# Kernel tuning notes

Hardware: AMD Instinct MI355X
Metric: run time of the kernel (lower is better)

The kernel has to match this reference:

```python
import jax, jax.numpy as jnp
import numpy as np

NUM_PERSISTENT = 16
ALIBI_ALPHA = 1.0
START_I = 0
DILATION = 1
LN_EPS = 1e-5


def setup_inputs() -> dict:
    key = jax.random.key(0)
    ks = jax.random.split(key, 16)
    B, S, C, H = 8, 1024, 512, 8
    D = C // H
    P = NUM_PERSISTENT
    Kk = 3
    x = jax.random.normal(ks[0], (B, S, C), dtype=jnp.float32)
    mask = jnp.ones((B, 1, S, S), dtype=jnp.int32)
    sc = 0.02
    Wq = jax.random.normal(ks[1], (D, D), jnp.float32) * sc
    Wk = jax.random.normal(ks[2], (D, D), jnp.float32) * sc
    Wv = jax.random.normal(ks[3], (D, D), jnp.float32) * sc
    pk = jax.random.normal(ks[4], (P, H, D), jnp.float32) * sc
    pv = jax.random.normal(ks[5], (P, H, D), jnp.float32) * sc
    th_pre = jax.random.normal(ks[6], (H, H), jnp.float32) * (1.0 / np.sqrt(H))
    th_post = jax.random.normal(ks[7], (H, H), jnp.float32) * (1.0 / np.sqrt(H))
    fc_w = jax.random.normal(ks[8], (C, C), jnp.float32) * sc
    fc_b = jnp.zeros((C,), jnp.float32)
    conv1_w = jax.random.normal(ks[9], (C, C, Kk), jnp.float32) * 0.01
    conv1_b = jnp.zeros((C,), jnp.float32)
    conv2_w = jax.random.normal(ks[10], (C, C, Kk), jnp.float32) * 0.01
    conv2_b = jnp.zeros((C,), jnp.float32)
    ln_g = jnp.ones((C,), jnp.float32)
    ln_b = jnp.zeros((C,), jnp.float32)
    return dict(x=x, mask=mask, Wq=Wq, Wk=Wk, Wv=Wv, pk=pk, pv=pv,
                th_pre=th_pre, th_post=th_post, fc_w=fc_w, fc_b=fc_b,
                conv1_w=conv1_w, conv1_b=conv1_b, conv2_w=conv2_w,
                conv2_b=conv2_b, ln_g=ln_g, ln_b=ln_b)


def _causal_conv(x_nct, w_oik, b_o, dilation):
    # padding (k-1)*d on both sides + chomp right == pad left only
    k = w_oik.shape[-1]
    p = (k - 1) * dilation
    y = jax.lax.conv_general_dilated(
        x_nct, w_oik, window_strides=(1,), padding=[(p, 0)],
        rhs_dilation=(dilation,), dimension_numbers=("NCH", "OIH", "NCH"))
    return y + b_o[None, :, None]


def reference(x, mask, Wq, Wk, Wv, pk, pv, th_pre, th_post, fc_w, fc_b,
              conv1_w, conv1_b, conv2_w, conv2_b, ln_g, ln_b):
    N, S, C = x.shape
    H = th_pre.shape[0]
    D = C // H
    P = pk.shape[0]

    # ---- MultiHeadAttention (eval: dropout = identity) ----
    xh = x.reshape(N, S, H, D)
    q = jnp.einsum("nshd,ed->nshe", xh, Wq)
    k = jnp.einsum("nshd,ed->nshe", xh, Wk)
    v = jnp.einsum("nshd,ed->nshe", xh, Wv)
    # persistent memory tokens appended along key/value length
    k = jnp.concatenate([k, jnp.broadcast_to(pk[None], (N, P, H, D))], axis=1)
    v = jnp.concatenate([v, jnp.broadcast_to(pv[None], (N, P, H, D))], axis=1)

    energy = jnp.einsum("nqhd,nkhd->nhqk", q, k)  # (N,H,S,S+P)

    # ALiBi bias (symmetric |q-k|), zero over persistent keys
    slopes = 2.0 ** (-(ALIBI_ALPHA * (jnp.arange(1, H + 1, dtype=jnp.float32) + START_I)))
    t = jnp.arange(S, dtype=jnp.float32)
    dist = jnp.abs(t[:, None] - t[None, :])  # (S,S)
    bias = -dist[None, None] * slopes[None, :, None, None]  # (1,H,S,S)
    bias = jnp.pad(bias, ((0, 0), (0, 0), (0, 0), (0, P)))
    energy = energy + bias

    # pre-softmax talking heads (1x1 conv over head axis)
    energy = jnp.einsum("hg,ngqk->nhqk", th_pre, energy)

    ext_mask = jnp.pad(mask, ((0, 0), (0, 0), (0, 0), (0, P)), constant_values=1)
    energy = jnp.where(ext_mask == 0, jnp.float32(-1e4), energy)

    attn = jax.nn.softmax(energy / jnp.sqrt(jnp.float32(C)), axis=-1)
    attn = jnp.einsum("hg,ngqk->nhqk", th_post, attn)

    att_out = jnp.einsum("nhql,nlhd->nqhd", attn, v).reshape(N, S, C)
    att_out = att_out @ fc_w.T + fc_b

    x = x + att_out  # residual (dropout1 identity in eval)

    # ---- TemporalBlock (causal dilated convs, no SE since heads>0) ----
    xc = jnp.transpose(x, (0, 2, 1))  # (N,C,S)
    h = jax.nn.relu(_causal_conv(xc, conv1_w, conv1_b, DILATION))
    h = jax.nn.relu(_causal_conv(h, conv2_w, conv2_b, DILATION))
    out = jax.nn.relu(h + xc)  # downsample is None (in==out)

    # mask out invalid frames
    conv_mask = mask[:, 0, :, 0][:, None, :]  # (N,1,S)
    out = jnp.where(conv_mask == 0, 0.0, out)

    y = jnp.transpose(out, (0, 2, 1))  # (N,S,C)
    mu = jnp.mean(y, axis=-1, keepdims=True)
    var = jnp.mean(jnp.square(y - mu), axis=-1, keepdims=True)
    y = (y - mu) * jax.lax.rsqrt(var + LN_EPS) * ln_g + ln_b
    return y
```

## Files before the change

kernel.cpp:

```cpp
#include <hip/hip_runtime.h>
#include <hip/hip_bf16.h>

#define BN 8
#define SS 1024
#define CC 512
#define HH 8
#define DD 64
#define PP 16
#define KT 1040

typedef __hip_bfloat16 bf16;
typedef unsigned char uchar;
typedef unsigned short ushort;
typedef unsigned int uint;
typedef __attribute__((ext_vector_type(8))) short short8;
typedef __attribute__((ext_vector_type(4))) float f32x4;
typedef __attribute__((ext_vector_type(2))) float f32x2;

__device__ __forceinline__ short f2s(float v){ bf16 b = __float2bfloat16(v); return *(short*)&b; }
__device__ __forceinline__ float s2f(short s){ bf16 b; *(short*)&b = s; return __bfloat162float(b); }
__device__ __forceinline__ uchar f2q(float v){
    return (uchar)__builtin_amdgcn_cvt_pk_fp8_f32(v, v, 0, false);
}

#define MFMA16(a,b,c)  __builtin_amdgcn_mfma_f32_16x16x32_bf16(a,b,c,0,0,0)
#define MFMAF8(a,b,c)  __builtin_amdgcn_mfma_f32_16x16x32_fp8_fp8(a,b,c,0,0,0)

__global__ __launch_bounds__(256) void prep_kernel(
    const float* __restrict__ fc_w, const float* __restrict__ c1w,
    const float* __restrict__ c2w, const float* __restrict__ Wq,
    const float* __restrict__ Wk, const float* __restrict__ Wv,
    const float* __restrict__ th_post,
    short* __restrict__ Bfc, uchar* __restrict__ Bc1,
    uchar* __restrict__ Bc2, short* __restrict__ Bqkv)
{
    int i = blockIdx.x*256 + threadIdx.x;
    const int NFC = 512*512, NCV = 512*1536, NQ = 3*64*64;
    if (i < NFC) {
        int c = i >> 9, r = i & 511;
        int g = r >> 6, d = r & 63;
        float s = 0.f;
        #pragma unroll
        for (int h = 0; h < 8; ++h)
            s += fc_w[(size_t)c*512 + h*64 + d] * th_post[h*8 + g];
        Bfc[i] = f2s(s);
        return;
    }
    i -= NFC;
    if (i < NCV) {
        int o = i/1536, r = i%1536, dk = r>>9, ci = r&511;
        Bc1[i] = f2q(c1w[(o*512+ci)*3+dk] * 16.f); return;
    }
    i -= NCV;
    if (i < NCV) {
        int o = i/1536, r = i%1536, dk = r>>9, ci = r&511;
        Bc2[i] = f2q(c2w[(o*512+ci)*3+dk] * 16.f); return;
    }
    i -= NCV;
    if (i < NQ) {
        int w = i >> 12, rest = i & 4095;
        const float* W = (w==0)?Wq:(w==1)?Wk:Wv;
        Bqkv[i] = f2s(W[((rest>>6)&63)*64 + (rest&63)]);
    }
}

__global__ __launch_bounds__(256) void qkv_mfma(
    const float* __restrict__ x, const short* __restrict__ Bqkv,
    uchar* __restrict__ qf, uchar* __restrict__ kf, uchar* __restrict__ vt)
{
    __shared__ short Xs[64*72];
    __shared__ short Ws[192*72];
    const int tid = threadIdx.x;
    const int m0 = blockIdx.x * 64;
    const int h = blockIdx.y;
    const int wave = tid >> 6, lane = tid & 63;
    const int lr = lane & 15, lq = lane >> 4;

    for (int i = tid; i < 1024; i += 256) {
        int r = i >> 4, cg = (i & 15)*4;
        float4 v = *(const float4*)(x + (size_t)(m0+r)*CC + h*64 + cg);
        Xs[r*72+cg+0] = f2s(v.x); Xs[r*72+cg+1] = f2s(v.y);
        Xs[r*72+cg+2] = f2s(v.z); Xs[r*72+cg+3] = f2s(v.w);
    }
    for (int i = tid; i < 3072; i += 256) {
        int r = i >> 4, cg = (i & 15)*4;
        *(short4*)(Ws + r*72 + cg) = *(const short4*)(Bqkv + (size_t)r*64 + cg);
    }
    __syncthreads();

    f32x4 acc[12];
    #pragma unroll
    for (int nt = 0; nt < 12; ++nt) acc[nt] = {0.f,0.f,0.f,0.f};
    #pragma unroll
    for (int ks = 0; ks < 2; ++ks) {
        int ko = ks*32 + lq*8;
        short8 a = *(const short8*)(Xs + (wave*16 + lr)*72 + ko);
        #pragma unroll
        for (int nt = 0; nt < 12; ++nt) {
            short8 b = *(const short8*)(Ws + (nt*16 + lr)*72 + ko);
            acc[nt] = MFMA16(a, b, acc[nt]);
        }
    }
    #pragma unroll
    for (int nt = 0; nt < 12; ++nt) {
        int ep = nt*16 + lr;
        int w = ep >> 6, e = ep & 63;
        #pragma unroll
        for (int reg = 0; reg < 4; ++reg) {
            int m = m0 + wave*16 + lq*4 + reg;
            int n = m >> 10, s = m & 1023;
            float v = acc[nt][reg];
            if (w == 0)      qf[((size_t)(n*HH+h)*SS + s)*DD + e] = f2q(v);
            else if (w == 1) kf[((size_t)(n*HH+h)*KT + s)*DD + e] = f2q(v);
            else             vt[(((size_t)(n*HH+h))*DD + e)*KT + s] = f2q(v);
        }
    }
}

__global__ __launch_bounds__(256) void persist_kernel(
    const float* __restrict__ pk, const float* __restrict__ pv,
    uchar* __restrict__ kf, uchar* __restrict__ vt)
{
    int idx = blockIdx.x*256 + threadIdx.x;
    if (idx >= BN*HH*PP*DD) return;
    int d = idx & 63, p = (idx >> 6) & 15, h = (idx >> 10) & 7, n = idx >> 13;
    size_t src = ((size_t)p*HH + h)*DD + d;
    kf[(((size_t)(n*HH+h))*KT + SS + p)*DD + d] = f2q(pk[src]);
    vt[(((size_t)(n*HH+h))*DD + d)*KT + SS + p] = f2q(pv[src]);
}

__device__ __forceinline__ void en_loadK(const uchar* __restrict__ kf,
    int nh, int kt, int tid, uint2* rk)
{
    #pragma unroll
    for (int j = 0; j < 2; ++j) {
        int i = tid + j*256;
        int r = i >> 3, c8 = (i & 7)*8;
        int kcol = kt*64 + r;
        uint2 v = {0u, 0u};
        if (kcol < KT)
            v = *(const uint2*)(kf + ((size_t)nh*KT + kcol)*DD + c8);
        rk[j] = v;
    }
}

__global__ __launch_bounds__(256) void energy_mfma8(
    const uchar* __restrict__ qf, const uchar* __restrict__ kf,
    uchar* __restrict__ E)
{
    __shared__ uchar Qs[64*72];
    __shared__ uchar Ks[64*72];
    const int tid = threadIdx.x;
    const int mt = blockIdx.x;
    const int nh = blockIdx.y;
    const int wave = tid >> 6, lane = tid & 63;
    const int lr = lane & 15, lq = lane >> 4;
    const int n = nh >> 3, h = nh & 7;

    #pragma unroll
    for (int j = 0; j < 2; ++j) {
        int i = tid + j*256;
        int r = i >> 3, c8 = (i & 7)*8;
        *(uint2*)(Qs + r*72 + c8) =
            *(const uint2*)(qf + ((size_t)nh*SS + mt*64 + r)*DD + c8);
    }

    uint2 rk[2];
    en_loadK(kf, nh, 0, tid, rk);

    for (int kt = 0; kt < 17; ++kt) {
        if (kt) __syncthreads();
        #pragma unroll
        for (int j = 0; j < 2; ++j) {
            int i = tid + j*256;
            *(uint2*)(Ks + (i >> 3)*72 + (i & 7)*8) = rk[j];
        }
        __syncthreads();
        if (kt + 1 < 17) en_loadK(kf, nh, kt+1, tid, rk);

        f32x4 acc[4];
        #pragma unroll
        for (int nt = 0; nt < 4; ++nt) acc[nt] = {0.f,0.f,0.f,0.f};
        #pragma unroll
        for (int ks = 0; ks < 2; ++ks) {
            int ko = ks*32 + lq*8;
            long a = *(const long*)(Qs + (wave*16 + lr)*72 + ko);
            #pragma unroll
            for (int nt = 0; nt < 4; ++nt) {
                long b = *(const long*)(Ks + (nt*16 + lr)*72 + ko);
                acc[nt] = MFMAF8(a, b, acc[nt]);
            }
        }
        #pragma unroll
        for (int nt = 0; nt < 4; ++nt) {
            int kcol = kt*64 + nt*16 + lr;
            if (kcol >= KT) continue;
            #pragma unroll
            for (int reg = 0; reg < 4; ++reg) {
                int q = mt*64 + wave*16 + lq*4 + reg;
                E[(((size_t)(n*SS + q))*HH + h)*KT + kcol] = f2q(acc[nt][reg]);
            }
        }
    }
}

__global__ __launch_bounds__(256) void softmax_kernel(
    uchar* __restrict__ E, const int* __restrict__ mask,
    const float* __restrict__ th_pre)
{
    __shared__ float thp[64];
    __shared__ float wred[4][8];
    const int tid = threadIdx.x;
    const int wave = tid >> 6, lane = tid & 63;
    const int blk = blockIdx.x;
    const int n = blk >> 10, q = blk & 1023;
    const float invs = 0.044194173824159216f;
    const float l2e  = 1.4426950408889634f;
    if (tid < 64) thp[tid] = th_pre[tid]*(invs*l2e);
    __syncthreads();
    uchar* Eb = E + (size_t)blk*HH*KT;

    const float sl[8] = {0.5f,0.25f,0.125f,0.0625f,
                         0.03125f,0.015625f,0.0078125f,0.00390625f};
    const int* mrow = mask + (size_t)n*SS*SS + (size_t)q*SS;

    const int k0 = tid*4;
    const int4 mk = *(const int4*)(mrow + k0);
    f32x4 dist;
    dist.x = fabsf((float)(q - k0));
    dist.y = fabsf((float)(q - k0 - 1));
    dist.z = fabsf((float)(q - k0 - 2));
    dist.w = fabsf((float)(q - k0 - 3));

    f32x4 tp[8];
    float tl[8];
    float sm[8];
    #pragma unroll
    for (int g = 0; g < 8; ++g) { sm[g] = 0.f; tl[g] = 0.f; }

    {
        f32x4 a[8];
        #pragma unroll
        for (int g = 0; g < 8; ++g) {
            uint u = *(const uint*)(Eb + g*KT + k0);
            f32x2 lo = __builtin_amdgcn_cvt_pk_f32_fp8((int)u, false);
            f32x2 hi = __builtin_amdgcn_cvt_pk_f32_fp8((int)u, true);
            f32x4 r; r.x = lo.x; r.y = lo.y; r.z = hi.x; r.w = hi.y;
            a[g] = r - dist*sl[g];
        }
        #pragma unroll
        for (int h = 0; h < 8; ++h) {
            f32x4 t = {0.f,0.f,0.f,0.f};
            #pragma unroll
            for (int g = 0; g < 8; ++g)
                t += a[g] * thp[h*8 + g];
            f32x4 e;
            e.x = (mk.x == 0) ? 0.f : exp2f(t.x);
            e.y = (mk.y == 0) ? 0.f : exp2f(t.y);
            e.z = (mk.z == 0) ? 0.f : exp2f(t.z);
            e.w = (mk.w == 0) ? 0.f : exp2f(t.w);
            tp[h] = e;
            sm[h] += e.x + e.y + e.z + e.w;
        }
    }
    if (tid < 16) {
        const int k = 1024 + tid;
        float a[8];
        #pragma unroll
        for (int g = 0; g < 8; ++g) {
            f32x2 r = __builtin_amdgcn_cvt_pk_f32_fp8((int)Eb[g*KT + k], false);
            a[g] = r.x;
        }
        #pragma unroll
        for (int h = 0; h < 8; ++h) {
            float t = 0.f;
            #pragma unroll
            for (int g = 0; g < 8; ++g) t = fmaf(thp[h*8 + g], a[g], t);
            float e = exp2f(t);
            tl[h] = e;
            sm[h] += e;
        }
    }
    #pragma unroll
    for (int g = 0; g < 8; ++g) {
        #pragma unroll
        for (int off = 32; off > 0; off >>= 1)
            sm[g] += __shfl_xor(sm[g], off);
    }
    if (lane == 0) {
        #pragma unroll
        for (int g = 0; g < 8; ++g) wred[wave][g] = sm[g];
    }
    __syncthreads();
    float lred[8];
    #pragma unroll
    for (int g = 0; g < 8; ++g)
        lred[g] = 1.0f / (wred[0][g] + wred[1][g] + wred[2][g] + wred[3][g]);

    #pragma unroll
    for (int h = 0; h < 8; ++h) {
        f32x4 e = tp[h] * lred[h];
        int p = __builtin_amdgcn_cvt_pk_fp8_f32(e.x, e.y, 0, false);
        p = __builtin_amdgcn_cvt_pk_fp8_f32(e.z, e.w, p, true);
        *(uint*)(Eb + h*KT + k0) = (uint)p;
    }
    if (tid < 16) {
        const int k = 1024 + tid;
        #pragma unroll
        for (int g = 0; g < 8; ++g)
            Eb[g*KT + k] = f2q(tl[g] * lred[g]);
    }
}

__device__ __forceinline__ void pv_loadP(const uchar* __restrict__ E,
    int n, int h, int ql0, int kt, int tid, uint2* rp)
{
    int r = tid >> 3, cg = (tid & 7)*8;
    int k = kt*64 + cg;
    uint2 v = {0u, 0u};
    if (k < KT)
        v = *(const uint2*)(E + (((size_t)(n*SS + ql0 + r))*HH + h)*KT + k);
    rp[0] = v;
}
__device__ __forceinline__ void pv_loadV(const uchar* __restrict__ vt,
    int nh, int kt, int tid, uint2* rv)
{
    #pragma unroll
    for (int j = 0; j < 2; ++j) {
        int i = tid + j*256;
        int r = i >> 3, cg = (i & 7)*8;
        int k = kt*64 + cg;
        uint2 v = {0u, 0u};
        if (k < KT)
            v = *(const uint2*)(vt + ((size_t)nh*DD + r)*KT + k);
        rv[j] = v;
    }
}

__global__ __launch_bounds__(256) void pv_mfma(
    const uchar* __restrict__ E, const uchar* __restrict__ vt,
    short* __restrict__ AO)
{
    __shared__ uchar Ps[32*72];
    __shared__ uchar Vs[64*72];
    const int tid = threadIdx.x;
    const int ql0 = blockIdx.x * 32;
    const int nh = blockIdx.y;
    const int n = nh >> 3, h = nh & 7;
    const int wave = tid >> 6, lane = tid & 63;
    const int lr = lane & 15, lq = lane >> 4;
    const int mh = wave & 1, nb = (wave >> 1)*32;

    uint2 rp[1], rv[2];
    pv_loadP(E, n, h, ql0, 0, tid, rp);
    pv_loadV(vt, nh, 0, tid, rv);

    f32x4 acc[2];
    acc[0] = {0.f,0.f,0.f,0.f}; acc[1] = {0.f,0.f,0.f,0.f};

    for (int kt = 0; kt < 17; ++kt) {
        if (kt) __syncthreads();
        {
            int r = tid >> 3, cg = (tid & 7)*8;
            *(uint2*)(Ps + r*72 + cg) = rp[0];
        }
        #pragma unroll
        for (int j = 0; j < 2; ++j) {
            int i = tid + j*256;
            *(uint2*)(Vs + (i >> 3)*72 + (i & 7)*8) = rv[j];
        }
        __syncthreads();
        if (kt + 1 < 17) {
            pv_loadP(E, n, h, ql0, kt+1, tid, rp);
            pv_loadV(vt, nh, kt+1, tid, rv);
        }
        #pragma unroll
        for (int ks = 0; ks < 2; ++ks) {
            int ko = ks*32 + lq*8;
            long a = *(const long*)(Ps + (mh*16 + lr)*72 + ko);
            #pragma unroll
            for (int nt = 0; nt < 2; ++nt) {
                long b = *(const long*)(Vs + (nb + nt*16 + lr)*72 + ko);
                acc[nt] = MFMAF8(a, b, acc[nt]);
            }
        }
    }
    #pragma unroll
    for (int nt = 0; nt < 2; ++nt) {
        int d = nb + nt*16 + lr;
        #pragma unroll
        for (int reg = 0; reg < 4; ++reg) {
            int qg = ql0 + mh*16 + lq*4 + reg;
            AO[((size_t)(n*SS) + qg)*CC + h*64 + d] = f2s(acc[nt][reg]);
        }
    }
}

__device__ __forceinline__ void g_load4(const short* __restrict__ src,
    size_t rowstride, int row0, int col0, int tid, short4* r)
{
    #pragma unroll
    for (int j = 0; j < 4; ++j) {
        int i = tid + j*256;
        int rr = i >> 4, cg = (i & 15)*4;
        r[j] = *(const short4*)(src + (size_t)(row0 + rr)*rowstride + col0 + cg);
    }
}
__device__ __forceinline__ void lds_store4(short* __restrict__ dst,
    int tid, const short4* r)
{
    #pragma unroll
    for (int j = 0; j < 4; ++j) {
        int i = tid + j*256;
        *(short4*)(dst + (i >> 4)*72 + (i & 15)*4) = r[j];
    }
}

__global__ __launch_bounds__(256) void fc_mfma(
    const short* __restrict__ A, const short* __restrict__ Bt,
    const float* __restrict__ bias, const float* __restrict__ x,
    short* __restrict__ out, uchar* __restrict__ out8)
{
    __shared__ short As[64*72];
    __shared__ short Bs[64*72];
    const int tid = threadIdx.x;
    const int lin = blockIdx.x + 8*blockIdx.y;
    const int xcd = lin & 7, slot = lin >> 3;
    const int m0 = (xcd*16 + (slot & 15))*64;
    const int n0 = (slot >> 4)*64;
    const int wave = tid >> 6, lane = tid & 63;
    const int lr = lane & 15, lq = lane >> 4;

    short4 ra[4], rb[4];
    g_load4(A, CC, m0, 0, tid, ra);
    g_load4(Bt, CC, n0, 0, tid, rb);

    f32x4 acc[4];
    #pragma unroll
    for (int nt = 0; nt < 4; ++nt) acc[nt] = {0.f,0.f,0.f,0.f};

    for (int kt = 0; kt < CC; kt += 64) {
        if (kt) __syncthreads();
        lds_store4(As, tid, ra);
        lds_store4(Bs, tid, rb);
        __syncthreads();
        if (kt + 64 < CC) {
            g_load4(A, CC, m0, kt+64, tid, ra);
            g_load4(Bt, CC, n0, kt+64, tid, rb);
        }
        #pragma unroll
        for (int ks = 0; ks < 2; ++ks) {
            int ko = ks*32 + lq*8;
            short8 a = *(const short8*)(As + (wave*16 + lr)*72 + ko);
            #pragma unroll
            for (int nt = 0; nt < 4; ++nt) {
                short8 b = *(const short8*)(Bs + (nt*16 + lr)*72 + ko);
                acc[nt] = MFMA16(a, b, acc[nt]);
            }
        }
    }
    #pragma unroll
    for (int nt = 0; nt < 4; ++nt) {
        int nn = n0 + nt*16 + lr;
        #pragma unroll
        for (int reg = 0; reg < 4; ++reg) {
            int m = m0 + wave*16 + lq*4 + reg;
            float v = acc[nt][reg] + bias[nn] + x[(size_t)m*CC + nn];
            out[(size_t)m*CC + nn]  = f2s(v);
            out8[(size_t)m*CC + nn] = f2q(v);
        }
    }
}

__device__ __forceinline__ void conv_loadA8(const uchar* __restrict__ A,
    int m0, int kt, int tid, uint2* ra)
{
    const int shift = (kt >> 9) - 2;
    const int ci0 = kt & 511;
    #pragma unroll
    for (int j = 0; j < 2; ++j) {
        int i = tid + j*256;
        int rr = i >> 3, c8 = (i & 7)*8;
        int m = m0 + rr;
        int s = m & (SS-1);
        uint2 v = {0u, 0u};
        if (s + shift >= 0)
            v = *(const uint2*)(A + (size_t)(m + shift)*CC + ci0 + c8);
        ra[j] = v;
    }
}
__device__ __forceinline__ void g_load8(const uchar* __restrict__ src,
    size_t rowstride, int row0, int col0, int tid, uint2* r)
{
    #pragma unroll
    for (int j = 0; j < 2; ++j) {
        int i = tid + j*256;
        int rr = i >> 3, c8 = (i & 7)*8;
        r[j] = *(const uint2*)(src + (size_t)(row0 + rr)*rowstride + col0 + c8);
    }
}
__device__ __forceinline__ void lds_store8(uchar* __restrict__ dst,
    int tid, const uint2* r)
{
    #pragma unroll
    for (int j = 0; j < 2; ++j) {
        int i = tid + j*256;
        *(uint2*)(dst + (i >> 3)*72 + (i & 7)*8) = r[j];
    }
}

__global__ __launch_bounds__(256) void conv_mfma8(
    const uchar* __restrict__ A, const uchar* __restrict__ Bt,
    const float* __restrict__ bias, uchar* __restrict__ out8,
    short* __restrict__ out16, int f8out)
{
    __shared__ uchar As[64*72];
    __shared__ uchar Bs[64*72];
    const int tid = threadIdx.x;
    const int lin = blockIdx.x + 8*blockIdx.y;
    const int xcd = lin & 7, slot = lin >> 3;
    const int m0 = (xcd*16 + (slot & 15))*64;
    const int n0 = (slot >> 4)*64;
    const int wave = tid >> 6, lane = tid & 63;
    const int lr = lane & 15, lq = lane >> 4;

    uint2 ra[2], rb[2];
    conv_loadA8(A, m0, 0, tid, ra);
    g_load8(Bt, 1536, n0, 0, tid, rb);

    f32x4 acc[4];
    #pragma unroll
    for (int nt = 0; nt < 4; ++nt) acc[nt] = {0.f,0.f,0.f,0.f};

    for (int kt = 0; kt < 1536; kt += 64) {
        if (kt) __syncthreads();
        lds_store8(As, tid, ra);
        lds_store8(Bs, tid, rb);
        __syncthreads();
        if (kt + 64 < 1536) {
            conv_loadA8(A, m0, kt+64, tid, ra);
            g_load8(Bt, 1536, n0, kt+64, tid, rb);
        }
        #pragma unroll
        for (int ks = 0; ks < 2; ++ks) {
            int ko = ks*32 + lq*8;
            long a = *(const long*)(As + (wave*16 + lr)*72 + ko);
            #pragma unroll
            for (int nt = 0; nt < 4; ++nt) {
                long b = *(const long*)(Bs + (nt*16 + lr)*72 + ko);
                acc[nt] = MFMAF8(a, b, acc[nt]);
            }
        }
    }
    #pragma unroll
    for (int nt = 0; nt < 4; ++nt) {
        int nn = n0 + nt*16 + lr;
        #pragma unroll
        for (int reg = 0; reg < 4; ++reg) {
            int m = m0 + wave*16 + lq*4 + reg;
            float v = fmaxf(acc[nt][reg]*0.0625f + bias[nn], 0.f);
            if (f8out) out8[(size_t)m*CC + nn]  = f2q(v);
            else       out16[(size_t)m*CC + nn] = f2s(v);
        }
    }
}

__global__ __launch_bounds__(256) void final_kernel(
    const short* __restrict__ c2, const short* __restrict__ xres,
    const int* __restrict__ mask, const float* __restrict__ g,
    const float* __restrict__ b, float* __restrict__ out)
{
    __shared__ float red[256];
    const int tid = threadIdx.x;
    const int m = blockIdx.x;
    const int n = m >> 10, s = m & 1023;
    const int mk = mask[(size_t)n*SS*SS + (size_t)s*SS];
    const int c0 = tid*2;

    short2 ca = *(const short2*)(c2 + (size_t)m*CC + c0);
    short2 xa = *(const short2*)(xres + (size_t)m*CC + c0);
    float v0 = fmaxf(s2f(ca.x) + s2f(xa.x), 0.f);
    float v1 = fmaxf(s2f(ca.y) + s2f(xa.y), 0.f);
    if (mk == 0) { v0 = 0.f; v1 = 0.f; }

    red[tid] = v0 + v1;
    __syncthreads();
    for (int off = 128; off > 0; off >>= 1) {
        if (tid < off) red[tid] += red[tid + off];
        __syncthreads();
    }
    float mu = red[0] * (1.0f/512.0f);
    __syncthreads();
    float d0 = v0 - mu, d1 = v1 - mu;
    red[tid] = d0*d0 + d1*d1;
    __syncthreads();
    for (int off = 128; off > 0; off >>= 1) {
        if (tid < off) red[tid] += red[tid + off];
        __syncthreads();
    }
    float rstd = rsqrtf(red[0] * (1.0f/512.0f) + 1e-5f);
    float2 gg = *(const float2*)(g + c0);
    float2 bb = *(const float2*)(b + c0);
    float2 o;
    o.x = d0*rstd*gg.x + bb.x;
    o.y = d1*rstd*gg.y + bb.y;
    *(float2*)(out + (size_t)m*CC + c0) = o;
}

extern "C" void kernel_launch(void* const* d_in, const int* in_sizes, int n_in,
                              void* d_out, int out_size, void* d_ws, size_t ws_size,
                              hipStream_t stream)
{
    const float* x      = (const float*)d_in[0];
    const int*   mask   = (const int*)  d_in[1];
    const float* Wq     = (const float*)d_in[2];
    const float* Wk     = (const float*)d_in[3];
    const float* Wv     = (const float*)d_in[4];
    const float* pk     = (const float*)d_in[5];
    const float* pv     = (const float*)d_in[6];
    const float* th_pre = (const float*)d_in[7];
    const float* th_post= (const float*)d_in[8];
    const float* fc_w   = (const float*)d_in[9];
    const float* fc_b   = (const float*)d_in[10];
    const float* c1w    = (const float*)d_in[11];
    const float* c1b    = (const float*)d_in[12];
    const float* c2w    = (const float*)d_in[13];
    const float* c2b    = (const float*)d_in[14];
    const float* lng    = (const float*)d_in[15];
    const float* lnb    = (const float*)d_in[16];
    float* out = (float*)d_out;
    (void)in_sizes; (void)n_in; (void)out_size; (void)ws_size;

    char* ws = (char*)d_ws;
    const size_t SZ_Q  = (size_t)BN*HH*SS*DD;
    const size_t SZ_K  = (size_t)BN*HH*KT*DD;
    const size_t SZ_VT = (size_t)BN*HH*DD*KT;
    const size_t SZ_E  = (size_t)BN*SS*HH*KT;
    const size_t SZ_A  = (size_t)BN*SS*CC*2;
    const size_t SZ_A8 = (size_t)BN*SS*CC;

    uchar* qf  = (uchar*)(ws);
    uchar* kf  = (uchar*)(ws + SZ_Q);
    uchar* vt  = (uchar*)(ws + SZ_Q + SZ_K);
    uchar* E   = (uchar*)(ws + SZ_Q + SZ_K + SZ_VT);
    short* AO  = (short*)(ws + SZ_Q + SZ_K + SZ_VT + SZ_E);
    char*  wend = ws + SZ_Q + SZ_K + SZ_VT + SZ_E + SZ_A;
    short* Bfc = (short*)(wend);
    uchar* Bc1 = (uchar*)(wend + 512*512*2);
    uchar* Bc2 = (uchar*)(wend + 512*512*2 + 512*1536);
    short* Bqkv= (short*)(wend + 512*512*2 + 2*512*1536);
    uchar* xres8 = (uchar*)(wend + 512*512*2 + 2*512*1536 + 3*64*64*2);
    short* c2buf = (short*)(wend + 512*512*2 + 2*512*1536 + 3*64*64*2 + SZ_A8);
    short* xres = (short*)(ws);
    uchar* h18  = (uchar*)E;

    {
        int total = 512*512 + 2*512*1536 + 3*64*64;
        prep_kernel<<<(total + 255)/256, 256, 0, stream>>>(
            fc_w, c1w, c2w, Wq, Wk, Wv, th_post, Bfc, Bc1, Bc2, Bqkv);
    }
    qkv_mfma<<<dim3(BN*SS/64, HH), 256, 0, stream>>>(x, Bqkv, qf, kf, vt);
    persist_kernel<<<(BN*HH*PP*DD + 255)/256, 256, 0, stream>>>(pk, pv, kf, vt);

    energy_mfma8<<<dim3(SS/64, BN*HH), 256, 0, stream>>>(qf, kf, E);
    softmax_kernel<<<BN*SS, 256, 0, stream>>>(E, mask, th_pre);
    pv_mfma<<<dim3(SS/32, BN*HH), 256, 0, stream>>>(E, vt, AO);

    fc_mfma<<<dim3(8, 128), 256, 0, stream>>>(AO, Bfc, fc_b, x, xres, xres8);
    conv_mfma8<<<dim3(8, 128), 256, 0, stream>>>(xres8, Bc1, c1b, h18, (short*)nullptr, 1);
    conv_mfma8<<<dim3(8, 128), 256, 0, stream>>>(h18, Bc2, c2b, (uchar*)nullptr, c2buf, 0);
    final_kernel<<<BN*SS, 256, 0, stream>>>(c2buf, xres, mask, lng, lnb, out);
}
```

Measured before the change: 298.6 us.

## Enlarge PV tile to 64 rows and double conv K-step to 128

Result: no change. 298.1 us (-0.2%).

```diff
diff --git a/kernel.cpp b/kernel.cpp
--- a/kernel.cpp
+++ b/kernel.cpp
@@ -315,12 +315,16 @@
 __device__ __forceinline__ void pv_loadP(const uchar* __restrict__ E,
     int n, int h, int ql0, int kt, int tid, uint2* rp)
 {
-    int r = tid >> 3, cg = (tid & 7)*8;
-    int k = kt*64 + cg;
-    uint2 v = {0u, 0u};
-    if (k < KT)
-        v = *(const uint2*)(E + (((size_t)(n*SS + ql0 + r))*HH + h)*KT + k);
-    rp[0] = v;
+    #pragma unroll
+    for (int j = 0; j < 2; ++j) {
+        int i = tid + j*256;
+        int r = i >> 3, cg = (i & 7)*8;
+        int k = kt*64 + cg;
+        uint2 v = {0u, 0u};
+        if (k < KT)
+            v = *(const uint2*)(E + (((size_t)(n*SS + ql0 + r))*HH + h)*KT + k);
+        rp[j] = v;
+    }
 }
 __device__ __forceinline__ void pv_loadV(const uchar* __restrict__ vt,
     int nh, int kt, int tid, uint2* rv)
@@ -341,28 +345,32 @@
     const uchar* __restrict__ E, const uchar* __restrict__ vt,
     short* __restrict__ AO)
 {
-    __shared__ uchar Ps[32*72];
+    __shared__ uchar Ps[64*72];
     __shared__ uchar Vs[64*72];
     const int tid = threadIdx.x;
-    const int ql0 = blockIdx.x * 32;
+    const int ql0 = blockIdx.x * 64;
     const int nh = blockIdx.y;
     const int n = nh >> 3, h = nh & 7;
     const int wave = tid >> 6, lane = tid & 63;
     const int lr = lane & 15, lq = lane >> 4;
-    const int mh = wave & 1, nb = (wave >> 1)*32;
-
-    uint2 rp[1], rv[2];
+    const int mq = (wave & 1)*32, nq = (wave >> 1)*32;
+
+    uint2 rp[2], rv[2];
     pv_loadP(E, n, h, ql0, 0, tid, rp);
     pv_loadV(vt, nh, 0, tid, rv);
 
-    f32x4 acc[2];
-    acc[0] = {0.f,0.f,0.f,0.f}; acc[1] = {0.f,0.f,0.f,0.f};
+    f32x4 acc[2][2];
+    #pragma unroll
+    for (int i = 0; i < 2; ++i)
+        #pragma unroll
+        for (int j = 0; j < 2; ++j) acc[i][j] = {0.f,0.f,0.f,0.f};
 
     for (int kt = 0; kt < 17; ++kt) {
         if (kt) __syncthreads();
-        {
-            int r = tid >> 3, cg = (tid & 7)*8;
-            *(uint2*)(Ps + r*72 + cg) = rp[0];
+        #pragma unroll
+        for (int j = 0; j < 2; ++j) {
+            int i = tid + j*256;
+            *(uint2*)(Ps + (i >> 3)*72 + (i & 7)*8) = rp[j];
         }
         #pragma unroll
         for (int j = 0; j < 2; ++j) {
@@ -377,23 +385,27 @@
         #pragma unroll
         for (int ks = 0; ks < 2; ++ks) {
             int ko = ks*32 + lq*8;
-            long a = *(const long*)(Ps + (mh*16 + lr)*72 + ko);
+            long a0 = *(const long*)(Ps + (mq + lr)*72 + ko);
+            long a1 = *(const long*)(Ps + (mq + 16 + lr)*72 + ko);
+            long b0 = *(const long*)(Vs + (nq + lr)*72 + ko);
+            long b1 = *(const long*)(Vs + (nq + 16 + lr)*72 + ko);
+            acc[0][0] = MFMAF8(a0, b0, acc[0][0]);
+            acc[0][1] = MFMAF8(a0, b1, acc[0][1]);
+            acc[1][0] = MFMAF8(a1, b0, acc[1][0]);
+            acc[1][1] = MFMAF8(a1, b1, acc[1][1]);
+        }
+    }
+    #pragma unroll
+    for (int mt = 0; mt < 2; ++mt)
+        #pragma unroll
+        for (int nt = 0; nt < 2; ++nt) {
+            int d = nq + nt*16 + lr;
             #pragma unroll
-            for (int nt = 0; nt < 2; ++nt) {
-                long b = *(const long*)(Vs + (nb + nt*16 + lr)*72 + ko);
-                acc[nt] = MFMAF8(a, b, acc[nt]);
+            for (int reg = 0; reg < 4; ++reg) {
+                int qg = ql0 + mq + mt*16 + lq*4 + reg;
+                AO[((size_t)(n*SS) + qg)*CC + h*64 + d] = f2s(acc[mt][nt][reg]);
             }
         }
-    }
-    #pragma unroll
-    for (int nt = 0; nt < 2; ++nt) {
-        int d = nb + nt*16 + lr;
-        #pragma unroll
-        for (int reg = 0; reg < 4; ++reg) {
-            int qg = ql0 + mh*16 + lq*4 + reg;
-            AO[((size_t)(n*SS) + qg)*CC + h*64 + d] = f2s(acc[nt][reg]);
-        }
-    }
 }
 
 __device__ __forceinline__ void g_load4(const short* __restrict__ src,
@@ -472,15 +484,15 @@
     }
 }
 
-__device__ __forceinline__ void conv_loadA8(const uchar* __restrict__ A,
+__device__ __forceinline__ void conv_loadA8w(const uchar* __restrict__ A,
     int m0, int kt, int tid, uint2* ra)
 {
     const int shift = (kt >> 9) - 2;
     const int ci0 = kt & 511;
     #pragma unroll
-    for (int j = 0; j < 2; ++j) {
-        int i = tid + j*256;
-        int rr = i >> 3, c8 = (i & 7)*8;
+    for (int j = 0; j < 4; ++j) {
+        int i = tid + j*256;
+        int rr = i >> 4, c8 = (i & 15)*8;
         int m = m0 + rr;
         int s = m & (SS-1);
         uint2 v = {0u, 0u};
@@ -489,23 +501,23 @@
         ra[j] = v;
     }
 }
-__device__ __forceinline__ void g_load8(const uchar* __restrict__ src,
+__device__ __forceinline__ void g_load8w(const uchar* __restrict__ src,
     size_t rowstride, int row0, int col0, int tid, uint2* r)
 {
     #pragma unroll
-    for (int j = 0; j < 2; ++j) {
-        int i = tid + j*256;
-        int rr = i >> 3, c8 = (i & 7)*8;
+    for (int j = 0; j < 4; ++j) {
+        int i = tid + j*256;
+        int rr = i >> 4, c8 = (i & 15)*8;
         r[j] = *(const uint2*)(src + (size_t)(row0 + rr)*rowstride + col0 + c8);
     }
 }
-__device__ __forceinline__ void lds_store8(uchar* __restrict__ dst,
+__device__ __forceinline__ void lds_store8w(uchar* __restrict__ dst,
     int tid, const uint2* r)
 {
     #pragma unroll
-    for (int j = 0; j < 2; ++j) {
-        int i = tid + j*256;
-        *(uint2*)(dst + (i >> 3)*72 + (i & 7)*8) = r[j];
+    for (int j = 0; j < 4; ++j) {
+        int i = tid + j*256;
+        *(uint2*)(dst + (i >> 4)*136 + (i & 15)*8) = r[j];
     }
 }
 
@@ -514,8 +526,8 @@
     const float* __restrict__ bias, uchar* __restrict__ out8,
     short* __restrict__ out16, int f8out)
 {
-    __shared__ uchar As[64*72];
-    __shared__ uchar Bs[64*72];
+    __shared__ uchar As[64*136];
+    __shared__ uchar Bs[64*136];
     const int tid = threadIdx.x;
     const int lin = blockIdx.x + 8*blockIdx.y;
     const int xcd = lin & 7, slot = lin >> 3;
@@ -524,30 +536,30 @@
     const int wave = tid >> 6, lane = tid & 63;
     const int lr = lane & 15, lq = lane >> 4;
 
-    uint2 ra[2], rb[2];
-    conv_loadA8(A, m0, 0, tid, ra);
-    g_load8(Bt, 1536, n0, 0, tid, rb);
+    uint2 ra[4], rb[4];
+    conv_loadA8w(A, m0, 0, tid, ra);
+    g_load8w(Bt, 1536, n0, 0, tid, rb);
 
     f32x4 acc[4];
     #pragma unroll
     for (int nt = 0; nt < 4; ++nt) acc[nt] = {0.f,0.f,0.f,0.f};
 
-    for (int kt = 0; kt < 1536; kt += 64) {
+    for (int kt = 0; kt < 1536; kt += 128) {
         if (kt) __syncthreads();
-        lds_store8(As, tid, ra);
-        lds_store8(Bs, tid, rb);
+        lds_store8w(As, tid, ra);
+        lds_store8w(Bs, tid, rb);
         __syncthreads();
-        if (kt + 64 < 1536) {
-            conv_loadA8(A, m0, kt+64, tid, ra);
-            g_load8(Bt, 1536, n0, kt+64, tid, rb);
-        }
-        #pragma unroll
-        for (int ks = 0; ks < 2; ++ks) {
+        if (kt + 128 < 1536) {
+            conv_loadA8w(A, m0, kt+128, tid, ra);
+            g_load8w(Bt, 1536, n0, kt+128, tid, rb);
+        }
+        #pragma unroll
+        for (int ks = 0; ks < 4; ++ks) {
             int ko = ks*32 + lq*8;
-            long a = *(const long*)(As + (wave*16 + lr)*72 + ko);
+            long a = *(const long*)(As + (wave*16 + lr)*136 + ko);
             #pragma unroll
             for (int nt = 0; nt < 4; ++nt) {
-                long b = *(const long*)(Bs + (nt*16 + lr)*72 + ko);
+                long b = *(const long*)(Bs + (nt*16 + lr)*136 + ko);
                 acc[nt] = MFMAF8(a, b, acc[nt]);
             }
         }
@@ -664,7 +676,7 @@
 
     energy_mfma8<<<dim3(SS/64, BN*HH), 256, 0, stream>>>(qf, kf, E);
     softmax_kernel<<<BN*SS, 256, 0, stream>>>(E, mask, th_pre);
-    pv_mfma<<<dim3(SS/32, BN*HH), 256, 0, stream>>>(E, vt, AO);
+    pv_mfma<<<dim3(SS/64, BN*HH), 256, 0, stream>>>(E, vt, AO);
 
     fc_mfma<<<dim3(8, 128), 256, 0, stream>>>(AO, Bfc, fc_b, x, xres, xres8);
     conv_mfma8<<<dim3(8, 128), 256, 0, stream>>>(xres8, Bc1, c1b, h18, (short*)nullptr, 1);
```
